# Kernel optimization log

Measured on AMD Instinct MI355X. Metric: run time of the kernel, lower is better.

The kernel has to match this reference:

```python
import jax, jax.numpy as jnp
import numpy as np

NUM_CLASSES = 10  # matches label fill_max; original iterates over train_label.unique()


def setup_inputs() -> dict:
    key = jax.random.key(0)
    k1, k2, k3 = jax.random.split(key, 3)
    n, m, d = 8192, 50000, 128
    x = jax.random.normal(k1, (n, d), dtype=jnp.float32)
    train_pts = jax.random.normal(k2, (m, d), dtype=jnp.float32)
    train_label = jax.random.randint(k3, (m,), 0, NUM_CLASSES, dtype=jnp.int32)
    return {"x": x, "train_pts": train_pts, "train_label": train_label, "k": 10}


def reference(x, train_pts, train_label, k):
    # Euclidean distance matrix [n, m]; same math as expand/pow/sum without the
    x2 = jnp.sum(x * x, axis=1, keepdims=True)          # [n, 1]
    y2 = jnp.sum(train_pts * train_pts, axis=1)         # [m]
    sq = x2 + y2[None, :] - 2.0 * (x @ train_pts.T)     # [n, m]
    dist = jnp.sqrt(jnp.maximum(sq, 0.0))
    # k smallest distances -> neighbor indices
    _, idx = jax.lax.top_k(-dist, k)                    # [n, k]
    votes = train_label[idx]                            # [n, k]
    # per-class vote counts; original loop: for lab in sorted unique labels,
    # who = count >= best -> ties go to the LARGEST label
    counts = jnp.sum(jax.nn.one_hot(votes, NUM_CLASSES, dtype=jnp.int32), axis=1)  # [n, C]
    winner = (NUM_CLASSES - 1) - jnp.argmax(counts[:, ::-1], axis=1)
    return winner.astype(train_label.dtype)
```

## Files before the change

### kernel.cpp

```cpp
#include <hip/hip_runtime.h>
#include <float.h>
#include <limits.h>

#define N_Q 8192
#define M_PTS 50000
#define DIM 128
#define KNN 10
#define NCLS 10
#define NCHUNK 16
#define TPC 196
#define CPC 8
#define NCAND (NCHUNK*CPC)
#define NSEL 24
#define TPL 6
#define QPB 128
#define SBIAS 256.0f
#define XN4 (N_Q*DIM/4)
#define YN4 (M_PTS*DIM/4)

typedef __attribute__((ext_vector_type(8))) int i32x8;
typedef __attribute__((ext_vector_type(4))) float f32x4;
typedef unsigned int u32;

__device__ __forceinline__ u32 pack4_e4m3(float4 v, float sc) {
    u32 w = 0;
    w = __builtin_amdgcn_cvt_pk_fp8_f32(sc * v.x, sc * v.y, w, false);
    w = __builtin_amdgcn_cvt_pk_fp8_f32(sc * v.z, sc * v.w, w, true);
    return w;
}

__global__ __launch_bounds__(256) void prep_kernel(
    const float4* __restrict__ x4, const float4* __restrict__ y4,
    u32* __restrict__ xb8, u32* __restrict__ yt8, float* __restrict__ y2) {
    int t = blockIdx.x * 256 + threadIdx.x;
    if (t < XN4) {
        xb8[t] = pack4_e4m3(x4[t], -2.0f);
    } else if (t < XN4 + YN4) {
        int j = t - XN4;
        int row = j >> 5;
        int d4  = j & 31;
        float4 v = y4[j];
        u32 w = pack4_e4m3(v, 1.0f);
        int T = row >> 4, nr = row & 15;
        int g2 = d4 >> 3, s = d4 & 7;
        yt8[(size_t)T * 512 + (g2 * 16 + nr) * 8 + s] = w;
        float p = v.x * v.x + v.y * v.y + v.z * v.z + v.w * v.w;
        #pragma unroll
        for (int off = 16; off > 0; off >>= 1) p += __shfl_xor(p, off, 64);
        if (d4 == 0) y2[row] = p + SBIAS;
    } else if (t < XN4 + YN4 + 176) {
        y2[M_PTS + (t - XN4 - YN4)] = FLT_MAX;
    }
}

__global__ __launch_bounds__(256, 4) void knn_filter(
    const u32* __restrict__ xb8, const u32* __restrict__ yt8,
    const float* __restrict__ y2, u32* __restrict__ ckey) {
    const int lane = threadIdx.x & 63;
    const int wid  = threadIdx.x >> 6;
    const int g    = lane >> 4;
    const int nrow = lane & 15;
    const int chunk = blockIdx.x;
    const int qb    = blockIdx.y;
    const int qw = qb * QPB + wid * 32;

    i32x8 bq0 = *(const i32x8*)(xb8 + (size_t)(qw + nrow) * 32 + g * 8);
    i32x8 bq1 = *(const i32x8*)(xb8 + (size_t)(qw + 16 + nrow) * 32 + g * 8);

    float ts0[TPL], ts1[TPL];
    #pragma unroll
    for (int l = 0; l < TPL; ++l) { ts0[l] = FLT_MAX; ts1[l] = FLT_MAX; }

    const u32* ytp = yt8 + (size_t)chunk * TPC * 512 + lane * 8;
    const f32x4* y2p = (const f32x4*)(y2 + chunk * TPC * 16 + g * 4);

    auto process = [&](i32x8 ay, f32x4 cq, int t) {
        f32x4 d0 = __builtin_amdgcn_mfma_scale_f32_16x16x128_f8f6f4(
            ay, bq0, cq, 0, 0, 0, 0x7F7F7F7F, 0, 0x7F7F7F7F);
        f32x4 d1 = __builtin_amdgcn_mfma_scale_f32_16x16x128_f8f6f4(
            ay, bq1, cq, 0, 0, 0, 0x7F7F7F7F, 0, 0x7F7F7F7F);
        u32 relb = (u32)(t * 16) | (u32)(g * 4);
        #pragma unroll
        for (int i = 0; i < 4; ++i) {
            float k0 = __uint_as_float((__float_as_uint(d0[i]) & 0xFFFFF000u) | (relb + i));
            float k1 = __uint_as_float((__float_as_uint(d1[i]) & 0xFFFFF000u) | (relb + i));
            float a0 = ts0[0], a1 = ts0[1], a2 = ts0[2], a3 = ts0[3], a4 = ts0[4];
            float b0 = ts1[0], b1 = ts1[1], b2 = ts1[2], b3 = ts1[3], b4 = ts1[4];
            ts0[0] = fminf(a0, k0);
            ts1[0] = fminf(b0, k1);
            ts0[1] = __builtin_amdgcn_fmed3f(k0, a0, a1);
            ts1[1] = __builtin_amdgcn_fmed3f(k1, b0, b1);
            ts0[2] = __builtin_amdgcn_fmed3f(k0, a1, a2);
            ts1[2] = __builtin_amdgcn_fmed3f(k1, b1, b2);
            ts0[3] = __builtin_amdgcn_fmed3f(k0, a2, a3);
            ts1[3] = __builtin_amdgcn_fmed3f(k1, b2, b3);
            ts0[4] = __builtin_amdgcn_fmed3f(k0, a3, a4);
            ts1[4] = __builtin_amdgcn_fmed3f(k1, b3, b4);
            ts0[5] = __builtin_amdgcn_fmed3f(k0, a4, ts0[5]);
            ts1[5] = __builtin_amdgcn_fmed3f(k1, b4, ts1[5]);
        }
    };

    i32x8 ayA = *(const i32x8*)(ytp);
    i32x8 ayB = *(const i32x8*)(ytp + 512);
    f32x4 cqA = y2p[0];
    f32x4 cqB = y2p[4];

    int t = 0;
    for (; t < TPC - 2; t += 2) {
        i32x8 nA = *(const i32x8*)(ytp + (size_t)(t + 2) * 512);
        f32x4 pA = y2p[(t + 2) * 4];
        process(ayA, cqA, t);
        ayA = nA; cqA = pA;
        i32x8 nB = *(const i32x8*)(ytp + (size_t)(t + 3) * 512);
        f32x4 pB = y2p[(t + 3) * 4];
        process(ayB, cqB, t + 1);
        ayB = nB; cqB = pB;
    }
    process(ayA, cqA, TPC - 2);
    process(ayB, cqB, TPC - 1);

    __shared__ u32 smem[QPB * 25];
    {
        int ql0 = wid * 32 + nrow;
        int ql1 = wid * 32 + 16 + nrow;
        #pragma unroll
        for (int l = 0; l < TPL; ++l) {
            smem[ql0 * 25 + g * TPL + l] = __float_as_uint(ts0[l]);
            smem[ql1 * 25 + g * TPL + l] = __float_as_uint(ts1[l]);
        }
    }
    __syncthreads();
    if (threadIdx.x < QPB) {
        int ql = threadIdx.x;
        float bs[CPC];
        #pragma unroll
        for (int i = 0; i < CPC; ++i) bs[i] = FLT_MAX;
        for (int e = 0; e < 4 * TPL; ++e) {
            float f = __uint_as_float(smem[ql * 25 + e]);
            #pragma unroll
            for (int q2 = 0; q2 < CPC; ++q2) {
                float mn = fminf(bs[q2], f);
                f = fmaxf(bs[q2], f);
                bs[q2] = mn;
            }
        }
        u32* dst = ckey + ((size_t)(qb * QPB + ql) * NCHUNK + chunk) * CPC;
        #pragma unroll
        for (int i = 0; i < CPC; ++i) dst[i] = __float_as_uint(bs[i]);
    }
}

__global__ __launch_bounds__(256) void knn_finalize(
    const u32* __restrict__ ckey, const float* __restrict__ x,
    const float* __restrict__ y, const int* __restrict__ labels,
    int* __restrict__ out) {
    const int lane = threadIdx.x & 63;
    const int wid  = threadIdx.x >> 6;
    const int qbase = blockIdx.x * 8;
    const int ql = wid * 2 + (lane >> 5);
    const int sl = lane & 31;

    __shared__ u32 skey[8][NCAND];
    __shared__ int sidx[8][NSEL];
    __shared__ double sex[8][NSEL];

    for (int i = threadIdx.x; i < 8 * NCAND; i += 256)
        skey[i >> 7][i & 127] = ckey[(size_t)(qbase + (i >> 7)) * NCAND + (i & 127)];
    __syncthreads();

    {
        u32 ke[4];
        int rank[4];
        #pragma unroll
        for (int r0 = 0; r0 < 4; ++r0) {
            ke[r0] = skey[ql][r0 * 32 + sl];
            rank[r0] = 0;
        }
        for (int j = 0; j < NCAND; ++j) {
            u32 kj = skey[ql][j];
            #pragma unroll
            for (int r0 = 0; r0 < 4; ++r0)
                rank[r0] += (kj < ke[r0] || (kj == ke[r0] && j < r0 * 32 + sl)) ? 1 : 0;
        }
        #pragma unroll
        for (int r0 = 0; r0 < 4; ++r0) {
            if (rank[r0] < NSEL) {
                int e = r0 * 32 + sl;
                sidx[ql][rank[r0]] = (e >> 3) * (TPC * 16) + (int)(ke[r0] & 0xFFFu);
            }
        }
    }
    __syncthreads();

    if (sl < NSEL) {
        const int idx = sidx[ql][sl];
        const float4* xr = (const float4*)(x + (size_t)(qbase + ql) * DIM);
        const float4* yr = (const float4*)(y + (size_t)idx * DIM);
        double dy2 = 0.0, dxy = 0.0;
        #pragma unroll 8
        for (int i = 0; i < 32; ++i) {
            float4 yv = yr[i];
            float4 xv = xr[i];
            dy2 = fma((double)yv.x, (double)yv.x, dy2);
            dy2 = fma((double)yv.y, (double)yv.y, dy2);
            dy2 = fma((double)yv.z, (double)yv.z, dy2);
            dy2 = fma((double)yv.w, (double)yv.w, dy2);
            dxy = fma((double)xv.x, (double)yv.x, dxy);
            dxy = fma((double)xv.y, (double)yv.y, dxy);
            dxy = fma((double)xv.z, (double)yv.z, dxy);
            dxy = fma((double)xv.w, (double)yv.w, dxy);
        }
        sex[ql][sl] = dy2 - 2.0 * dxy;
    }
    __syncthreads();

    if (sl == 0) {
        double tsv[KNN]; int ti[KNN];
        #pragma unroll
        for (int i = 0; i < KNN; ++i) { tsv[i] = 1e300; ti[i] = INT_MAX; }
        #pragma unroll
        for (int c = 0; c < NSEL; ++c) {
            double s = sex[ql][c];
            int id = sidx[ql][c];
            #pragma unroll
            for (int pp = 0; pp < KNN; ++pp) {
                bool lt = (s < tsv[pp]) || (s == tsv[pp] && id < ti[pp]);
                double ns = lt ? tsv[pp] : s;  int nid = lt ? ti[pp] : id;
                tsv[pp] = lt ? s : tsv[pp];    ti[pp] = lt ? id : ti[pp];
                s = ns; id = nid;
            }
        }
        int lab[KNN];
        #pragma unroll
        for (int i = 0; i < KNN; ++i) lab[i] = labels[ti[i]];
        int bestc = 0, bestn = -1;
        #pragma unroll
        for (int c = 0; c < NCLS; ++c) {
            int n = 0;
            #pragma unroll
            for (int i = 0; i < KNN; ++i) n += (lab[i] == c) ? 1 : 0;
            if (n >= bestn) { bestn = n; bestc = c; }
        }
        out[qbase + ql] = bestc;
    }
}

extern "C" void kernel_launch(void* const* d_in, const int* in_sizes, int n_in,
                              void* d_out, int out_size, void* d_ws, size_t ws_size,
                              hipStream_t stream) {
    const float* x      = (const float*)d_in[0];
    const float* y      = (const float*)d_in[1];
    const int*   labels = (const int*)d_in[2];

    char* ws = (char*)d_ws;
    size_t off = 0;
    u32* xb8 = (u32*)(ws + off);    off += (size_t)N_Q * DIM;
    u32* yt8 = (u32*)(ws + off);    off += (size_t)NCHUNK * TPC * 2048;
    float* y2 = (float*)(ws + off); off += (size_t)NCHUNK * TPC * 16 * 4;
    u32* ckey = (u32*)(ws + off);   off += (size_t)N_Q * NCAND * 4;
    int* out = (int*)d_out;

    prep_kernel<<<(XN4 + YN4 + 176 + 255) / 256, 256, 0, stream>>>(
        (const float4*)x, (const float4*)y, xb8, yt8, y2);
    knn_filter<<<dim3(NCHUNK, N_Q / QPB), 256, 0, stream>>>(xb8, yt8, y2, ckey);
    knn_finalize<<<N_Q / 8, 256, 0, stream>>>(ckey, x, y, labels, out);
}
```

Before: 268.2 us.

## Swap MFMA operand roles so each lane tracks per-query top-4 lists

The filter kernel swaps the A/B operands of the fp8 MFMA so that query rows land in the output rows and training points in the columns. Each lane then keeps eight per-query top-4 lists instead of two top-6 lists, which cuts the fmed3 insertion chain per key. The shared-memory merge grows from 24 to 64 candidates per query, with a 65-word row stride. In finalize, the dot-product loop is split across four independent double accumulators, and the serial top-10 insertion done by one lane is replaced by a parallel rank count across 24 lanes. The shorter per-lane lists risk dropping true neighbours if several fall into the same lane.

Result: faster. 226.2 us (-15.7%).

```diff
diff --git a/kernel.cpp b/kernel.cpp
--- a/kernel.cpp
+++ b/kernel.cpp
@@ -12,7 +12,7 @@
 #define CPC 8
 #define NCAND (NCHUNK*CPC)
 #define NSEL 24
-#define TPL 6
+#define TPL 4
 #define QPB 128
 #define SBIAS 256.0f
 #define XN4 (N_Q*DIM/4)
@@ -64,80 +64,68 @@
     const int qb    = blockIdx.y;
     const int qw = qb * QPB + wid * 32;
 
-    i32x8 bq0 = *(const i32x8*)(xb8 + (size_t)(qw + nrow) * 32 + g * 8);
-    i32x8 bq1 = *(const i32x8*)(xb8 + (size_t)(qw + 16 + nrow) * 32 + g * 8);
-
-    float ts0[TPL], ts1[TPL];
+    i32x8 a[2];
     #pragma unroll
-    for (int l = 0; l < TPL; ++l) { ts0[l] = FLT_MAX; ts1[l] = FLT_MAX; }
+    for (int s = 0; s < 2; ++s)
+        a[s] = *(const i32x8*)(xb8 + (size_t)(qw + s * 16 + nrow) * 32 + g * 8);
+
+    float ts[8][TPL];
+    #pragma unroll
+    for (int r = 0; r < 8; ++r)
+        #pragma unroll
+        for (int l = 0; l < TPL; ++l) ts[r][l] = FLT_MAX;
 
     const u32* ytp = yt8 + (size_t)chunk * TPC * 512 + lane * 8;
-    const f32x4* y2p = (const f32x4*)(y2 + chunk * TPC * 16 + g * 4);
-
-    auto process = [&](i32x8 ay, f32x4 cq, int t) {
+    const float* y2p = y2 + chunk * TPC * 16 + nrow;
+
+    #pragma unroll 2
+    for (int t = 0; t < TPC; ++t) {
+        i32x8 b = *(const i32x8*)(ytp + (size_t)t * 512);
+        float y2n = y2p[t * 16];
+        f32x4 cq = {y2n, y2n, y2n, y2n};
         f32x4 d0 = __builtin_amdgcn_mfma_scale_f32_16x16x128_f8f6f4(
-            ay, bq0, cq, 0, 0, 0, 0x7F7F7F7F, 0, 0x7F7F7F7F);
+            a[0], b, cq, 0, 0, 0, 0x7F7F7F7F, 0, 0x7F7F7F7F);
         f32x4 d1 = __builtin_amdgcn_mfma_scale_f32_16x16x128_f8f6f4(
-            ay, bq1, cq, 0, 0, 0, 0x7F7F7F7F, 0, 0x7F7F7F7F);
-        u32 relb = (u32)(t * 16) | (u32)(g * 4);
+            a[1], b, cq, 0, 0, 0, 0x7F7F7F7F, 0, 0x7F7F7F7F);
+        u32 rel = (u32)(t * 16) | (u32)nrow;
         #pragma unroll
         for (int i = 0; i < 4; ++i) {
-            float k0 = __uint_as_float((__float_as_uint(d0[i]) & 0xFFFFF000u) | (relb + i));
-            float k1 = __uint_as_float((__float_as_uint(d1[i]) & 0xFFFFF000u) | (relb + i));
-            float a0 = ts0[0], a1 = ts0[1], a2 = ts0[2], a3 = ts0[3], a4 = ts0[4];
-            float b0 = ts1[0], b1 = ts1[1], b2 = ts1[2], b3 = ts1[3], b4 = ts1[4];
-            ts0[0] = fminf(a0, k0);
-            ts1[0] = fminf(b0, k1);
-            ts0[1] = __builtin_amdgcn_fmed3f(k0, a0, a1);
-            ts1[1] = __builtin_amdgcn_fmed3f(k1, b0, b1);
-            ts0[2] = __builtin_amdgcn_fmed3f(k0, a1, a2);
-            ts1[2] = __builtin_amdgcn_fmed3f(k1, b1, b2);
-            ts0[3] = __builtin_amdgcn_fmed3f(k0, a2, a3);
-            ts1[3] = __builtin_amdgcn_fmed3f(k1, b2, b3);
-            ts0[4] = __builtin_amdgcn_fmed3f(k0, a3, a4);
-            ts1[4] = __builtin_amdgcn_fmed3f(k1, b3, b4);
-            ts0[5] = __builtin_amdgcn_fmed3f(k0, a4, ts0[5]);
-            ts1[5] = __builtin_amdgcn_fmed3f(k1, b4, ts1[5]);
-        }
-    };
-
-    i32x8 ayA = *(const i32x8*)(ytp);
-    i32x8 ayB = *(const i32x8*)(ytp + 512);
-    f32x4 cqA = y2p[0];
-    f32x4 cqB = y2p[4];
-
-    int t = 0;
-    for (; t < TPC - 2; t += 2) {
-        i32x8 nA = *(const i32x8*)(ytp + (size_t)(t + 2) * 512);
-        f32x4 pA = y2p[(t + 2) * 4];
-        process(ayA, cqA, t);
-        ayA = nA; cqA = pA;
-        i32x8 nB = *(const i32x8*)(ytp + (size_t)(t + 3) * 512);
-        f32x4 pB = y2p[(t + 3) * 4];
-        process(ayB, cqB, t + 1);
-        ayB = nB; cqB = pB;
-    }
-    process(ayA, cqA, TPC - 2);
-    process(ayB, cqB, TPC - 1);
-
-    __shared__ u32 smem[QPB * 25];
-    {
-        int ql0 = wid * 32 + nrow;
-        int ql1 = wid * 32 + 16 + nrow;
-        #pragma unroll
-        for (int l = 0; l < TPL; ++l) {
-            smem[ql0 * 25 + g * TPL + l] = __float_as_uint(ts0[l]);
-            smem[ql1 * 25 + g * TPL + l] = __float_as_uint(ts1[l]);
-        }
-    }
+            float key = __uint_as_float((__float_as_uint(d0[i]) & 0xFFFFF000u) | rel);
+            float o0 = ts[i][0], o1 = ts[i][1], o2 = ts[i][2];
+            ts[i][0] = fminf(o0, key);
+            ts[i][1] = __builtin_amdgcn_fmed3f(key, o0, o1);
+            ts[i][2] = __builtin_amdgcn_fmed3f(key, o1, o2);
+            ts[i][3] = __builtin_amdgcn_fmed3f(key, o2, ts[i][3]);
+        }
+        #pragma unroll
+        for (int i = 0; i < 4; ++i) {
+            float key = __uint_as_float((__float_as_uint(d1[i]) & 0xFFFFF000u) | rel);
+            float o0 = ts[4 + i][0], o1 = ts[4 + i][1], o2 = ts[4 + i][2];
+            ts[4 + i][0] = fminf(o0, key);
+            ts[4 + i][1] = __builtin_amdgcn_fmed3f(key, o0, o1);
+            ts[4 + i][2] = __builtin_amdgcn_fmed3f(key, o1, o2);
+            ts[4 + i][3] = __builtin_amdgcn_fmed3f(key, o2, ts[4 + i][3]);
+        }
+    }
+
+    __shared__ u32 smem[QPB * 65];
+    #pragma unroll
+    for (int s = 0; s < 2; ++s)
+        #pragma unroll
+        for (int r = 0; r < 4; ++r) {
+            int ql = wid * 32 + s * 16 + g * 4 + r;
+            #pragma unroll
+            for (int l = 0; l < TPL; ++l)
+                smem[ql * 65 + nrow * TPL + l] = __float_as_uint(ts[s * 4 + r][l]);
+        }
     __syncthreads();
     if (threadIdx.x < QPB) {
         int ql = threadIdx.x;
         float bs[CPC];
         #pragma unroll
         for (int i = 0; i < CPC; ++i) bs[i] = FLT_MAX;
-        for (int e = 0; e < 4 * TPL; ++e) {
-            float f = __uint_as_float(smem[ql * 25 + e]);
+        for (int e = 0; e < 16 * TPL; ++e) {
+            float f = __uint_as_float(smem[ql * 65 + e]);
             #pragma unroll
             for (int q2 = 0; q2 < CPC; ++q2) {
                 float mn = fminf(bs[q2], f);
@@ -164,6 +152,7 @@
     __shared__ u32 skey[8][NCAND];
     __shared__ int sidx[8][NSEL];
     __shared__ double sex[8][NSEL];
+    __shared__ int slab[8][KNN];
 
     for (int i = threadIdx.x; i < 8 * NCAND; i += 256)
         skey[i >> 7][i & 127] = ckey[(size_t)(qbase + (i >> 7)) * NCAND + (i & 127)];
@@ -193,47 +182,48 @@
     }
     __syncthreads();
 
+    int myidx = 0;
     if (sl < NSEL) {
-        const int idx = sidx[ql][sl];
+        myidx = sidx[ql][sl];
         const float4* xr = (const float4*)(x + (size_t)(qbase + ql) * DIM);
-        const float4* yr = (const float4*)(y + (size_t)idx * DIM);
-        double dy2 = 0.0, dxy = 0.0;
-        #pragma unroll 8
+        const float4* yr = (const float4*)(y + (size_t)myidx * DIM);
+        double dy[4] = {0.0, 0.0, 0.0, 0.0};
+        double dx[4] = {0.0, 0.0, 0.0, 0.0};
+        #pragma unroll
         for (int i = 0; i < 32; ++i) {
             float4 yv = yr[i];
             float4 xv = xr[i];
-            dy2 = fma((double)yv.x, (double)yv.x, dy2);
-            dy2 = fma((double)yv.y, (double)yv.y, dy2);
-            dy2 = fma((double)yv.z, (double)yv.z, dy2);
-            dy2 = fma((double)yv.w, (double)yv.w, dy2);
-            dxy = fma((double)xv.x, (double)yv.x, dxy);
-            dxy = fma((double)xv.y, (double)yv.y, dxy);
-            dxy = fma((double)xv.z, (double)yv.z, dxy);
-            dxy = fma((double)xv.w, (double)yv.w, dxy);
-        }
-        sex[ql][sl] = dy2 - 2.0 * dxy;
+            int k = i & 3;
+            dy[k] = fma((double)yv.x, (double)yv.x, dy[k]);
+            dy[k] = fma((double)yv.y, (double)yv.y, dy[k]);
+            dy[k] = fma((double)yv.z, (double)yv.z, dy[k]);
+            dy[k] = fma((double)yv.w, (double)yv.w, dy[k]);
+            dx[k] = fma((double)xv.x, (double)yv.x, dx[k]);
+            dx[k] = fma((double)xv.y, (double)yv.y, dx[k]);
+            dx[k] = fma((double)xv.z, (double)yv.z, dx[k]);
+            dx[k] = fma((double)xv.w, (double)yv.w, dx[k]);
+        }
+        sex[ql][sl] = ((dy[0] + dy[1]) + (dy[2] + dy[3]))
+                    - 2.0 * ((dx[0] + dx[1]) + (dx[2] + dx[3]));
+    }
+    __syncthreads();
+
+    if (sl < NSEL) {
+        double s = sex[ql][sl];
+        int cnt = 0;
+        #pragma unroll
+        for (int j = 0; j < NSEL; ++j) {
+            double sj = sex[ql][j];
+            cnt += (sj < s || (sj == s && sidx[ql][j] < myidx)) ? 1 : 0;
+        }
+        if (cnt < KNN) slab[ql][cnt] = labels[myidx];
     }
     __syncthreads();
 
     if (sl == 0) {
-        double tsv[KNN]; int ti[KNN];
-        #pragma unroll
-        for (int i = 0; i < KNN; ++i) { tsv[i] = 1e300; ti[i] = INT_MAX; }
-        #pragma unroll
-        for (int c = 0; c < NSEL; ++c) {
-            double s = sex[ql][c];
-            int id = sidx[ql][c];
-            #pragma unroll
-            for (int pp = 0; pp < KNN; ++pp) {
-                bool lt = (s < tsv[pp]) || (s == tsv[pp] && id < ti[pp]);
-                double ns = lt ? tsv[pp] : s;  int nid = lt ? ti[pp] : id;
-                tsv[pp] = lt ? s : tsv[pp];    ti[pp] = lt ? id : ti[pp];
-                s = ns; id = nid;
-            }
-        }
         int lab[KNN];
         #pragma unroll
-        for (int i = 0; i < KNN; ++i) lab[i] = labels[ti[i]];
+        for (int i = 0; i < KNN; ++i) lab[i] = slab[ql][i];
         int bestc = 0, bestn = -1;
         #pragma unroll
         for (int c = 0; c < NCLS; ++c) {
```
